# Kernel optimization log

Measured on AMD Instinct MI355X. Metric: run time of the kernel, lower is better.

Reference implementation:

```python
import jax, jax.numpy as jnp
import numpy as np

N = 524288          # number of query points
L_FREQ = 16         # frequencies in positional encoding -> dim_encoding = 3*2*16 = 96
DIM_ENC = 96
DIM_HID = 128
NUM_LAYERS = 8      # 1 input layer + 7 hidden layers + 1 output layer
DIM_OUT = 4
DIM_IN_HID = DIM_HID + DIM_ENC  # concat skip: 224


def setup_inputs() -> dict:
    key = jax.random.key(0)
    ks = jax.random.split(key, 7)
    def lin(k, fan_in, shape):
        return jax.random.uniform(k, shape, jnp.float32, -1.0, 1.0) / np.sqrt(fan_in)
    return {
        "query_points": jax.random.uniform(ks[0], (N, 3), jnp.float32),
        "W0": lin(ks[1], DIM_ENC, (DIM_ENC, DIM_HID)),
        "b0": lin(ks[2], DIM_ENC, (DIM_HID,)),
        "Wh": lin(ks[3], DIM_IN_HID, (NUM_LAYERS - 1, DIM_IN_HID, DIM_HID)),
        "bh": lin(ks[4], DIM_IN_HID, (NUM_LAYERS - 1, DIM_HID)),
        "Wl": lin(ks[5], DIM_IN_HID, (DIM_IN_HID, DIM_OUT)),
        "bl": lin(ks[6], DIM_IN_HID, (DIM_OUT,)),
    }


def _encode(x):
    # NeRF frequency encoding: [N,3] -> [N, 3*2*L_FREQ]
    freqs = (2.0 ** jnp.arange(L_FREQ, dtype=x.dtype)) * jnp.pi
    xf = x[..., None] * freqs                      # [N, 3, L]
    enc = jnp.concatenate([jnp.sin(xf), jnp.cos(xf)], axis=-1)  # [N, 3, 2L]
    return enc.reshape(x.shape[0], -1)             # [N, 96]


def reference(query_points, W0, b0, Wh, bh, Wl, bl):
    enc = _encode(query_points)                    # [N, 96]
    outs = jnp.maximum(enc @ W0 + b0, 0.0)         # [N, 128]
    outs = jnp.concatenate([outs, enc], axis=-1)   # concat skip -> [N, 224]
    for i in range(Wh.shape[0]):                   # 7 structurally-distinct hidden layers
        outs = jnp.maximum(outs @ Wh[i] + bh[i], 0.0)
        outs = jnp.concatenate([outs, enc], axis=-1)
    return outs @ Wl + bl                          # [N, 4], no activation on last layer
```

## Files before the change

### kernel.cpp

```cpp
#include <hip/hip_runtime.h>
#include <stdint.h>

typedef unsigned short u16;
typedef __bf16 bf16x8 __attribute__((ext_vector_type(8)));
typedef float f32x4 __attribute__((ext_vector_type(4)));
typedef unsigned int u32;

#define IMG_L0 0
#define IMG_H(l) (16384 + ((l)-1) * 32768)
#define IMG_OUT 245760
#define IMG_TOTAL 249856

__device__ inline int sinv(int q) {
    int s = q >> 5, gg = (q >> 3) & 3, u = (q >> 2) & 1, t = q & 3;
    return 16 * (2 * s + u) + 4 * gg + t;
}
__device__ inline int encmap(int q) {
    int c = q >> 5, gg = (q >> 3) & 3, u = (q >> 2) & 1, t = q & 3;
    int trig = gg >> 1, freq = 8 * (gg & 1) + 4 * u + t;
    return c * 32 + trig * 16 + freq;
}
__device__ inline u16 b16rne(float v) {
    u32 u = __builtin_bit_cast(u32, v);
    u += 0x7FFFu + ((u >> 16) & 1u);
    return (u16)(u >> 16);
}

__global__ void nf_prep(const float* __restrict__ W0, const float* __restrict__ b0,
                        const float* __restrict__ Wh, const float* __restrict__ bh,
                        const float* __restrict__ Wl, const float* __restrict__ bl,
                        u16* __restrict__ img) {
    int idx = blockIdx.x * 256 + threadIdx.x;
    if (idx >= IMG_TOTAL) return;
    int kpos, i, R, base;
    float v;
    if (idx < 16384) {
        kpos = idx >> 7; i = idx & 127; R = 128; base = IMG_L0;
        v = (kpos < 96) ? W0[encmap(kpos) * 128 + i]
          : (kpos == 96) ? b0[i] : 0.f;
    } else if (idx < IMG_OUT) {
        int r = idx - 16384; int l = r >> 15; int rr = r & 32767;
        kpos = rr >> 7; i = rr & 127; R = 128; base = 16384 + l * 32768;
        const float* W = Wh + l * 224 * 128;
        v = (kpos < 128) ? W[sinv(kpos) * 128 + i]
          : (kpos < 224) ? W[(128 + encmap(kpos - 128)) * 128 + i]
          : (kpos == 224) ? bh[l * 128 + i] : 0.f;
    } else {
        int r = idx - IMG_OUT; kpos = r >> 4; i = r & 15; R = 16; base = IMG_OUT;
        v = 0.f;
        if (i < 4) {
            v = (kpos < 128) ? Wl[sinv(kpos) * 4 + i]
              : (kpos < 224) ? Wl[(128 + encmap(kpos - 128)) * 4 + i]
              : (kpos == 224) ? bl[i] : 0.f;
        }
    }
    img[base + (((kpos >> 3) * R + i) << 3) + (kpos & 7)] = b16rne(v);
}

__device__ inline f32x4 MF(bf16x8 a, bf16x8 b, f32x4 c) {
    return __builtin_amdgcn_mfma_f32_16x16x32_bf16(a, b, c, 0, 0, 0);
}
__device__ inline bf16x8 fr4(const u32 (&p)[4]) {
    union { u32 u[4]; bf16x8 v; } x;
    x.u[0] = p[0]; x.u[1] = p[1]; x.u[2] = p[2]; x.u[3] = p[3];
    return x.v;
}
__device__ inline bf16x8 frCB(u32 c0) {
    union { u32 u[4]; bf16x8 v; } x;
    x.u[0] = c0; x.u[1] = 0; x.u[2] = 0; x.u[3] = 0;
    return x.v;
}
__device__ inline bf16x8 ldA(const u16* base, int gi) {
    union { uint4 q; bf16x8 v; } x;
    x.q = *(const uint4*)(base + (gi << 3));
    return x.v;
}
__device__ inline u32 pkbf(float a, float b) {
    u32 ua = __builtin_bit_cast(u32, a) + 0x8000u;
    u32 ub = __builtin_bit_cast(u32, b) + 0x8000u;
    return __builtin_amdgcn_perm(ub, ua, 0x07060302u);
}
__device__ inline void stageA(const u16* gsrc, u16* ldst, int bytes, int wave, int lane) {
    const char* gs = (const char*)gsrc + lane * 16;
    char* ls = (char*)ldst;
    for (int c = wave * 1024; c < bytes; c += 8192)
        __builtin_amdgcn_global_load_lds(
            (const __attribute__((address_space(1))) void*)(gs + c),
            (__attribute__((address_space(3))) void*)(ls + c), 16, 0, 0);
}
__device__ inline void zeroacc(f32x4 (&acc)[8][2]) {
#pragma unroll
    for (int T = 0; T < 8; T++) {
        acc[T][0] = f32x4{0.f, 0.f, 0.f, 0.f};
        acc[T][1] = f32x4{0.f, 0.f, 0.f, 0.f};
    }
}
__device__ inline void buildH(const f32x4 (&acc)[8][2], u32 (&H)[2][4][4]) {
#pragma unroll
    for (int n = 0; n < 2; n++)
#pragma unroll
        for (int s = 0; s < 4; s++) {
            f32x4 a = acc[2 * s][n], b = acc[2 * s + 1][n];
            float a0 = fmaxf(a[0], 0.f), a1 = fmaxf(a[1], 0.f);
            float a2 = fmaxf(a[2], 0.f), a3 = fmaxf(a[3], 0.f);
            float c0 = fmaxf(b[0], 0.f), c1 = fmaxf(b[1], 0.f);
            float c2 = fmaxf(b[2], 0.f), c3 = fmaxf(b[3], 0.f);
            H[n][s][0] = pkbf(a0, a1); H[n][s][1] = pkbf(a2, a3);
            H[n][s][2] = pkbf(c0, c1); H[n][s][3] = pkbf(c2, c3);
        }
}
template <int HALF>
__device__ inline void compute_l0(const u16* A, int g, int m, f32x4 (&acc)[8][2],
                                  const u32 (&E)[2][3][4], u32 CB0) {
#pragma unroll
    for (int sr = 0; sr < 2; sr++) {
        const int s = HALF * 2 + sr;
        bf16x8 B0, B1;
        if (s < 3) { B0 = fr4(E[0][s]); B1 = fr4(E[1][s]); }
        else       { B0 = frCB(CB0);    B1 = B0; }
#pragma unroll
        for (int T = 0; T < 8; T++) {
            bf16x8 a = ldA(A, (4 * sr + g) * 128 + 16 * T + m);
            acc[T][0] = MF(a, B0, acc[T][0]);
            acc[T][1] = MF(a, B1, acc[T][1]);
        }
    }
}
template <int HALF>
__device__ inline void compute_half(const u16* A, int g, int m, f32x4 (&acc)[8][2],
                                    const u32 (&H)[2][4][4], const u32 (&E)[2][3][4],
                                    u32 CB0) {
#pragma unroll
    for (int sr = 0; sr < 4; sr++) {
        const int s = HALF * 4 + sr;
        bf16x8 B0, B1;
        if (s < 4)      { B0 = fr4(H[0][s]);     B1 = fr4(H[1][s]); }
        else if (s < 7) { B0 = fr4(E[0][s - 4]); B1 = fr4(E[1][s - 4]); }
        else            { B0 = frCB(CB0);        B1 = B0; }
#pragma unroll
        for (int T = 0; T < 8; T++) {
            bf16x8 a = ldA(A, (4 * sr + g) * 128 + 16 * T + m);
            acc[T][0] = MF(a, B0, acc[T][0]);
            acc[T][1] = MF(a, B1, acc[T][1]);
        }
    }
}

__global__ __launch_bounds__(512, 2) void nf_main(const float* __restrict__ qp,
                                                  const u16* __restrict__ img,
                                                  float* __restrict__ out) {
    __shared__ alignas(16) u16 lds[2][16384];
    const int tid = threadIdx.x, wave = tid >> 6, lane = tid & 63;
    const int m = lane & 15, g = lane >> 4;
    const int pbase = blockIdx.x * 256 + wave * 32;

    stageA(img + IMG_L0, &lds[0][0], 16384, wave, lane);

    float xs[2][3];
#pragma unroll
    for (int c = 0; c < 3; c++) {
        xs[0][c] = qp[(pbase + m) * 3 + c];
        xs[1][c] = qp[(pbase + 16 + m) * 3 + c];
    }
    u32 E[2][3][4];
    const float sc0 = (g & 1) ? 128.0f : 0.5f;
    const bool iscos = (g & 2);
#pragma unroll
    for (int n = 0; n < 2; n++)
#pragma unroll
        for (int c = 0; c < 3; c++) {
            float r = xs[n][c] * sc0;
            float v[8];
#pragma unroll
            for (int t = 0; t < 8; t++) {
                float fr = __builtin_amdgcn_fractf(r);
                v[t] = iscos ? __builtin_amdgcn_cosf(fr) : __builtin_amdgcn_sinf(fr);
                r = r * 2.0f;
            }
            E[n][c][0] = pkbf(v[0], v[1]); E[n][c][1] = pkbf(v[2], v[3]);
            E[n][c][2] = pkbf(v[4], v[5]); E[n][c][3] = pkbf(v[6], v[7]);
        }
    const u32 CB0 = (g == 0) ? 0x00003F80u : 0u;
    f32x4 acc[8][2];
    u32 H[2][4][4];
    zeroacc(acc);

    __syncthreads();
    stageA(img + IMG_L0 + 8192, &lds[1][0], 16384, wave, lane);
    compute_l0<0>(&lds[0][0], g, m, acc, E, CB0);
    __syncthreads();
    stageA(img + IMG_H(1), &lds[0][0], 32768, wave, lane);
    compute_l0<1>(&lds[1][0], g, m, acc, E, CB0);
    buildH(acc, H);
    __syncthreads();

#pragma unroll 1
    for (int l = 1; l < 8; l++) {
        const int ibase = IMG_H(l);
        stageA(img + ibase + 16384, &lds[1][0], 32768, wave, lane);
        zeroacc(acc);
        compute_half<0>(&lds[0][0], g, m, acc, H, E, CB0);
        __syncthreads();
        const u16* nsrc = (l < 7) ? (img + ibase + 32768) : (img + IMG_OUT);
        stageA(nsrc, &lds[0][0], (l < 7) ? 32768 : 8192, wave, lane);
        compute_half<1>(&lds[1][0], g, m, acc, H, E, CB0);
        buildH(acc, H);
        __syncthreads();
    }

    f32x4 o0 = {0.f, 0.f, 0.f, 0.f}, o1 = {0.f, 0.f, 0.f, 0.f};
#pragma unroll
    for (int s = 0; s < 8; s++) {
        bf16x8 B0, B1;
        if (s < 4)      { B0 = fr4(H[0][s]);     B1 = fr4(H[1][s]); }
        else if (s < 7) { B0 = fr4(E[0][s - 4]); B1 = fr4(E[1][s - 4]); }
        else            { B0 = frCB(CB0);        B1 = B0; }
        bf16x8 a = ldA(&lds[0][0], (4 * s + g) * 16 + m);
        o0 = MF(a, B0, o0);
        o1 = MF(a, B1, o1);
    }
    if (g == 0) {
        *(f32x4*)(out + 4 * (pbase + m))      = o0;
        *(f32x4*)(out + 4 * (pbase + 16 + m)) = o1;
    }
}

extern "C" void kernel_launch(void* const* d_in, const int* in_sizes, int n_in,
                              void* d_out, int out_size, void* d_ws, size_t ws_size,
                              hipStream_t stream) {
    const float* qp = (const float*)d_in[0];
    const float* W0 = (const float*)d_in[1];
    const float* b0 = (const float*)d_in[2];
    const float* Wh = (const float*)d_in[3];
    const float* bh = (const float*)d_in[4];
    const float* Wl = (const float*)d_in[5];
    const float* bl = (const float*)d_in[6];
    float* out = (float*)d_out;
    u16* img = (u16*)d_ws;

    nf_prep<<<976, 256, 0, stream>>>(W0, b0, Wh, bh, Wl, bl, img);
    nf_main<<<2048, 512, 0, stream>>>(qp, img, out);
}
```

Before: 308.8 us.

## Double per-wave point tile and recompute encoding instead of caching it

Each wave now handles 64 points (four 16-point MFMA tiles) instead of 32, and blocks shrink to 4 waves of 256 threads, so every weight fragment read from LDS feeds twice as many MFMAs. To keep register pressure in check, the encoding fragments are no longer held in registers. They are recomputed with sin/cos for every layer. The trade is more transcendental ALU work and more accumulator registers in exchange for half the LDS traffic per MFMA and more weight staging per wave.

```diff
diff --git a/kernel.cpp b/kernel.cpp
--- a/kernel.cpp
+++ b/kernel.cpp
@@ -5,6 +5,8 @@
 typedef __bf16 bf16x8 __attribute__((ext_vector_type(8)));
 typedef float f32x4 __attribute__((ext_vector_type(4)));
 typedef unsigned int u32;
+
+#define NT 4
 
 #define IMG_L0 0
 #define IMG_H(l) (16384 + ((l)-1) * 32768)
@@ -80,117 +82,140 @@
     u32 ub = __builtin_bit_cast(u32, b) + 0x8000u;
     return __builtin_amdgcn_perm(ub, ua, 0x07060302u);
 }
+__device__ inline bf16x8 encFrag(float x, float sc0, bool iscos) {
+    float r = x * sc0;
+    float v[8];
+#pragma unroll
+    for (int t = 0; t < 8; t++) {
+        float fr = __builtin_amdgcn_fractf(r);
+        v[t] = iscos ? __builtin_amdgcn_cosf(fr) : __builtin_amdgcn_sinf(fr);
+        r = r * 2.0f;
+    }
+    union { u32 u[4]; bf16x8 v; } o;
+    o.u[0] = pkbf(v[0], v[1]); o.u[1] = pkbf(v[2], v[3]);
+    o.u[2] = pkbf(v[4], v[5]); o.u[3] = pkbf(v[6], v[7]);
+    return o.v;
+}
 __device__ inline void stageA(const u16* gsrc, u16* ldst, int bytes, int wave, int lane) {
     const char* gs = (const char*)gsrc + lane * 16;
     char* ls = (char*)ldst;
-    for (int c = wave * 1024; c < bytes; c += 8192)
+    for (int c = wave * 1024; c < bytes; c += 4096)
         __builtin_amdgcn_global_load_lds(
             (const __attribute__((address_space(1))) void*)(gs + c),
             (__attribute__((address_space(3))) void*)(ls + c), 16, 0, 0);
 }
-__device__ inline void zeroacc(f32x4 (&acc)[8][2]) {
-#pragma unroll
-    for (int T = 0; T < 8; T++) {
-        acc[T][0] = f32x4{0.f, 0.f, 0.f, 0.f};
-        acc[T][1] = f32x4{0.f, 0.f, 0.f, 0.f};
-    }
-}
-__device__ inline void buildH(const f32x4 (&acc)[8][2], u32 (&H)[2][4][4]) {
-#pragma unroll
-    for (int n = 0; n < 2; n++)
+__device__ inline void zeroacc(f32x4 (&acc)[8][NT]) {
+#pragma unroll
+    for (int T = 0; T < 8; T++)
+#pragma unroll
+        for (int n = 0; n < NT; n++)
+            acc[T][n] = f32x4{0.f, 0.f, 0.f, 0.f};
+}
+__device__ inline void buildH(const f32x4 (&acc)[8][NT], u32 (&H)[NT][4][4]) {
+#pragma unroll
+    for (int n = 0; n < NT; n++)
 #pragma unroll
         for (int s = 0; s < 4; s++) {
             f32x4 a = acc[2 * s][n], b = acc[2 * s + 1][n];
-            float a0 = fmaxf(a[0], 0.f), a1 = fmaxf(a[1], 0.f);
-            float a2 = fmaxf(a[2], 0.f), a3 = fmaxf(a[3], 0.f);
-            float c0 = fmaxf(b[0], 0.f), c1 = fmaxf(b[1], 0.f);
-            float c2 = fmaxf(b[2], 0.f), c3 = fmaxf(b[3], 0.f);
-            H[n][s][0] = pkbf(a0, a1); H[n][s][1] = pkbf(a2, a3);
-            H[n][s][2] = pkbf(c0, c1); H[n][s][3] = pkbf(c2, c3);
+            H[n][s][0] = pkbf(fmaxf(a[0], 0.f), fmaxf(a[1], 0.f));
+            H[n][s][1] = pkbf(fmaxf(a[2], 0.f), fmaxf(a[3], 0.f));
+            H[n][s][2] = pkbf(fmaxf(b[0], 0.f), fmaxf(b[1], 0.f));
+            H[n][s][3] = pkbf(fmaxf(b[2], 0.f), fmaxf(b[3], 0.f));
         }
 }
 template <int HALF>
-__device__ inline void compute_l0(const u16* A, int g, int m, f32x4 (&acc)[8][2],
-                                  const u32 (&E)[2][3][4], u32 CB0) {
+__device__ inline void computeL0(const u16* A, int g, int m, f32x4 (&acc)[8][NT],
+                                 const float (&xs)[NT][3], float sc0, bool iscos,
+                                 u32 CB0) {
 #pragma unroll
     for (int sr = 0; sr < 2; sr++) {
         const int s = HALF * 2 + sr;
-        bf16x8 B0, B1;
-        if (s < 3) { B0 = fr4(E[0][s]); B1 = fr4(E[1][s]); }
-        else       { B0 = frCB(CB0);    B1 = B0; }
+        bf16x8 B[NT];
+        if (s < 3) {
+#pragma unroll
+            for (int n = 0; n < NT; n++) B[n] = encFrag(xs[n][s], sc0, iscos);
+        } else {
+            bf16x8 cb = frCB(CB0);
+#pragma unroll
+            for (int n = 0; n < NT; n++) B[n] = cb;
+        }
 #pragma unroll
         for (int T = 0; T < 8; T++) {
             bf16x8 a = ldA(A, (4 * sr + g) * 128 + 16 * T + m);
-            acc[T][0] = MF(a, B0, acc[T][0]);
-            acc[T][1] = MF(a, B1, acc[T][1]);
-        }
-    }
-}
-template <int HALF>
-__device__ inline void compute_half(const u16* A, int g, int m, f32x4 (&acc)[8][2],
-                                    const u32 (&H)[2][4][4], const u32 (&E)[2][3][4],
-                                    u32 CB0) {
+#pragma unroll
+            for (int n = 0; n < NT; n++) acc[T][n] = MF(a, B[n], acc[T][n]);
+        }
+    }
+}
+__device__ inline void computeHalf0(const u16* A, int g, int m, f32x4 (&acc)[8][NT],
+                                    const u32 (&H)[NT][4][4]) {
 #pragma unroll
     for (int sr = 0; sr < 4; sr++) {
-        const int s = HALF * 4 + sr;
-        bf16x8 B0, B1;
-        if (s < 4)      { B0 = fr4(H[0][s]);     B1 = fr4(H[1][s]); }
-        else if (s < 7) { B0 = fr4(E[0][s - 4]); B1 = fr4(E[1][s - 4]); }
-        else            { B0 = frCB(CB0);        B1 = B0; }
+        bf16x8 B[NT];
+#pragma unroll
+        for (int n = 0; n < NT; n++) B[n] = fr4(H[n][sr]);
 #pragma unroll
         for (int T = 0; T < 8; T++) {
             bf16x8 a = ldA(A, (4 * sr + g) * 128 + 16 * T + m);
-            acc[T][0] = MF(a, B0, acc[T][0]);
-            acc[T][1] = MF(a, B1, acc[T][1]);
-        }
-    }
-}
-
-__global__ __launch_bounds__(512, 2) void nf_main(const float* __restrict__ qp,
+#pragma unroll
+            for (int n = 0; n < NT; n++) acc[T][n] = MF(a, B[n], acc[T][n]);
+        }
+    }
+}
+__device__ inline void computeHalf1(const u16* A, int g, int m, f32x4 (&acc)[8][NT],
+                                    const float (&xs)[NT][3], float sc0, bool iscos,
+                                    u32 CB0) {
+#pragma unroll
+    for (int sr = 0; sr < 4; sr++) {
+        bf16x8 B[NT];
+        if (sr < 3) {
+#pragma unroll
+            for (int n = 0; n < NT; n++) B[n] = encFrag(xs[n][sr], sc0, iscos);
+        } else {
+            bf16x8 cb = frCB(CB0);
+#pragma unroll
+            for (int n = 0; n < NT; n++) B[n] = cb;
+        }
+#pragma unroll
+        for (int T = 0; T < 8; T++) {
+            bf16x8 a = ldA(A, (4 * sr + g) * 128 + 16 * T + m);
+#pragma unroll
+            for (int n = 0; n < NT; n++) acc[T][n] = MF(a, B[n], acc[T][n]);
+        }
+    }
+}
+
+__global__ __launch_bounds__(256, 2) void nf_main(const float* __restrict__ qp,
                                                   const u16* __restrict__ img,
                                                   float* __restrict__ out) {
     __shared__ alignas(16) u16 lds[2][16384];
     const int tid = threadIdx.x, wave = tid >> 6, lane = tid & 63;
     const int m = lane & 15, g = lane >> 4;
-    const int pbase = blockIdx.x * 256 + wave * 32;
+    const int pbase = blockIdx.x * 256 + wave * 64;
 
     stageA(img + IMG_L0, &lds[0][0], 16384, wave, lane);
 
-    float xs[2][3];
-#pragma unroll
-    for (int c = 0; c < 3; c++) {
-        xs[0][c] = qp[(pbase + m) * 3 + c];
-        xs[1][c] = qp[(pbase + 16 + m) * 3 + c];
-    }
-    u32 E[2][3][4];
+    float xs[NT][3];
+#pragma unroll
+    for (int n = 0; n < NT; n++)
+#pragma unroll
+        for (int c = 0; c < 3; c++)
+            xs[n][c] = qp[(pbase + n * 16 + m) * 3 + c];
+
     const float sc0 = (g & 1) ? 128.0f : 0.5f;
     const bool iscos = (g & 2);
-#pragma unroll
-    for (int n = 0; n < 2; n++)
-#pragma unroll
-        for (int c = 0; c < 3; c++) {
-            float r = xs[n][c] * sc0;
-            float v[8];
-#pragma unroll
-            for (int t = 0; t < 8; t++) {
-                float fr = __builtin_amdgcn_fractf(r);
-                v[t] = iscos ? __builtin_amdgcn_cosf(fr) : __builtin_amdgcn_sinf(fr);
-                r = r * 2.0f;
-            }
-            E[n][c][0] = pkbf(v[0], v[1]); E[n][c][1] = pkbf(v[2], v[3]);
-            E[n][c][2] = pkbf(v[4], v[5]); E[n][c][3] = pkbf(v[6], v[7]);
-        }
     const u32 CB0 = (g == 0) ? 0x00003F80u : 0u;
-    f32x4 acc[8][2];
-    u32 H[2][4][4];
+
+    f32x4 acc[8][NT];
+    u32 H[NT][4][4];
     zeroacc(acc);
 
     __syncthreads();
     stageA(img + IMG_L0 + 8192, &lds[1][0], 16384, wave, lane);
-    compute_l0<0>(&lds[0][0], g, m, acc, E, CB0);
+    computeL0<0>(&lds[0][0], g, m, acc, xs, sc0, iscos, CB0);
     __syncthreads();
     stageA(img + IMG_H(1), &lds[0][0], 32768, wave, lane);
-    compute_l0<1>(&lds[1][0], g, m, acc, E, CB0);
+    computeL0<1>(&lds[1][0], g, m, acc, xs, sc0, iscos, CB0);
     buildH(acc, H);
     __syncthreads();
 
@@ -199,29 +224,40 @@
         const int ibase = IMG_H(l);
         stageA(img + ibase + 16384, &lds[1][0], 32768, wave, lane);
         zeroacc(acc);
-        compute_half<0>(&lds[0][0], g, m, acc, H, E, CB0);
+        computeHalf0(&lds[0][0], g, m, acc, H);
         __syncthreads();
         const u16* nsrc = (l < 7) ? (img + ibase + 32768) : (img + IMG_OUT);
         stageA(nsrc, &lds[0][0], (l < 7) ? 32768 : 8192, wave, lane);
-        compute_half<1>(&lds[1][0], g, m, acc, H, E, CB0);
+        computeHalf1(&lds[1][0], g, m, acc, xs, sc0, iscos, CB0);
         buildH(acc, H);
         __syncthreads();
     }
 
-    f32x4 o0 = {0.f, 0.f, 0.f, 0.f}, o1 = {0.f, 0.f, 0.f, 0.f};
+    f32x4 o[NT];
+#pragma unroll
+    for (int n = 0; n < NT; n++) o[n] = f32x4{0.f, 0.f, 0.f, 0.f};
 #pragma unroll
     for (int s = 0; s < 8; s++) {
-        bf16x8 B0, B1;
-        if (s < 4)      { B0 = fr4(H[0][s]);     B1 = fr4(H[1][s]); }
-        else if (s < 7) { B0 = fr4(E[0][s - 4]); B1 = fr4(E[1][s - 4]); }
-        else            { B0 = frCB(CB0);        B1 = B0; }
+        bf16x8 B[NT];
+        if (s < 4) {
+#pragma unroll
+            for (int n = 0; n < NT; n++) B[n] = fr4(H[n][s]);
+        } else if (s < 7) {
+#pragma unroll
+            for (int n = 0; n < NT; n++) B[n] = encFrag(xs[n][s - 4], sc0, iscos);
+        } else {
+            bf16x8 cb = frCB(CB0);
+#pragma unroll
+            for (int n = 0; n < NT; n++) B[n] = cb;
+        }
         bf16x8 a = ldA(&lds[0][0], (4 * s + g) * 16 + m);
-        o0 = MF(a, B0, o0);
-        o1 = MF(a, B1, o1);
+#pragma unroll
+        for (int n = 0; n < NT; n++) o[n] = MF(a, B[n], o[n]);
     }
     if (g == 0) {
-        *(f32x4*)(out + 4 * (pbase + m))      = o0;
-        *(f32x4*)(out + 4 * (pbase + 16 + m)) = o1;
+#pragma unroll
+        for (int n = 0; n < NT; n++)
+            *(f32x4*)(out + 4 * (pbase + n * 16 + m)) = o[n];
     }
 }
 
@@ -239,5 +275,5 @@
     u16* img = (u16*)d_ws;
 
     nf_prep<<<976, 256, 0, stream>>>(W0, b0, Wh, bh, Wl, bl, img);
-    nf_main<<<2048, 512, 0, stream>>>(qp, img, out);
-}
+    nf_main<<<2048, 256, 0, stream>>>(qp, img, out);
+}
```

After: 267.1 us. -13.5%, faster.

## Switch MLP to 32x32x16 MFMA with 64-point waves and tighter weight image

Applied to the files above, without the earlier changes.

Replaces the 16x16x32 bf16 MFMA tiling with 32x32x16 MFMA, so each wave handles 64 points and blocks shrink to 256 threads. Each lane now computes both sin and cos for its encoding slice. The weight image is repacked with a new K-permutation that drops padding rows (224+bias instead of 256 per layer). The aim is to cut LDS A-operand reads per FLOP and wasted K padding, at the cost of more accumulator registers and fewer waves per block.

```diff
diff --git a/kernel.cpp b/kernel.cpp
--- a/kernel.cpp
+++ b/kernel.cpp
@@ -4,21 +4,16 @@
 typedef unsigned short u16;
 typedef __bf16 bf16x8 __attribute__((ext_vector_type(8)));
 typedef float f32x4 __attribute__((ext_vector_type(4)));
+typedef float f32x16 __attribute__((ext_vector_type(16)));
 typedef unsigned int u32;
 
-#define IMG_L0 0
-#define IMG_H(l) (16384 + ((l)-1) * 32768)
-#define IMG_OUT 245760
-#define IMG_TOTAL 249856
-
-__device__ inline int sinv(int q) {
-    int s = q >> 5, gg = (q >> 3) & 3, u = (q >> 2) & 1, t = q & 3;
-    return 16 * (2 * s + u) + 4 * gg + t;
-}
-__device__ inline int encmap(int q) {
-    int c = q >> 5, gg = (q >> 3) & 3, u = (q >> 2) & 1, t = q & 3;
-    int trig = gg >> 1, freq = 8 * (gg & 1) + 4 * u + t;
-    return c * 32 + trig * 16 + freq;
+#define IMG_H(l) (14336 + ((l)-1) * 30720)
+#define IMG_OUT 229376
+#define IMG_TOTAL 237056
+
+__device__ inline int fmap(int k) {
+    int s = k >> 4, h = (k >> 3) & 1, j = k & 7;
+    return 32 * (s >> 1) + 16 * (s & 1) + 8 * (j >> 2) + 4 * h + (j & 3);
 }
 __device__ inline u16 b16rne(float v) {
     u32 u = __builtin_bit_cast(u32, v);
@@ -32,33 +27,35 @@
                         u16* __restrict__ img) {
     int idx = blockIdx.x * 256 + threadIdx.x;
     if (idx >= IMG_TOTAL) return;
-    int kpos, i, R, base;
     float v;
-    if (idx < 16384) {
-        kpos = idx >> 7; i = idx & 127; R = 128; base = IMG_L0;
-        v = (kpos < 96) ? W0[encmap(kpos) * 128 + i]
-          : (kpos == 96) ? b0[i] : 0.f;
+    if (idx < 14336) {
+        int gg = idx >> 3, j = idx & 7;
+        int koct = gg >> 7, i = gg & 127, k = koct * 8 + j;
+        v = (k < 96) ? W0[k * 128 + i] : (k == 96) ? b0[i] : 0.f;
     } else if (idx < IMG_OUT) {
-        int r = idx - 16384; int l = r >> 15; int rr = r & 32767;
-        kpos = rr >> 7; i = rr & 127; R = 128; base = 16384 + l * 32768;
+        int r = idx - 14336, l = r / 30720, rr = r % 30720;
+        int gg = rr >> 3, j = rr & 7;
+        int koct = gg >> 7, i = gg & 127, k = koct * 8 + j;
         const float* W = Wh + l * 224 * 128;
-        v = (kpos < 128) ? W[sinv(kpos) * 128 + i]
-          : (kpos < 224) ? W[(128 + encmap(kpos - 128)) * 128 + i]
-          : (kpos == 224) ? bh[l * 128 + i] : 0.f;
+        v = (k < 128) ? W[fmap(k) * 128 + i]
+          : (k < 224) ? W[k * 128 + i]
+          : (k == 224) ? bh[l * 128 + i] : 0.f;
     } else {
-        int r = idx - IMG_OUT; kpos = r >> 4; i = r & 15; R = 16; base = IMG_OUT;
+        int r = idx - IMG_OUT;
+        int gg = r >> 3, j = r & 7;
+        int koct = gg >> 5, i = gg & 31, k = koct * 8 + j;
         v = 0.f;
-        if (i < 4) {
-            v = (kpos < 128) ? Wl[sinv(kpos) * 4 + i]
-              : (kpos < 224) ? Wl[(128 + encmap(kpos - 128)) * 4 + i]
-              : (kpos == 224) ? bl[i] : 0.f;
-        }
-    }
-    img[base + (((kpos >> 3) * R + i) << 3) + (kpos & 7)] = b16rne(v);
-}
-
-__device__ inline f32x4 MF(bf16x8 a, bf16x8 b, f32x4 c) {
-    return __builtin_amdgcn_mfma_f32_16x16x32_bf16(a, b, c, 0, 0, 0);
+        if (i < 4)
+            v = (k < 128) ? Wl[fmap(k) * 4 + i]
+              : (k < 224) ? Wl[k * 4 + i]
+              : (k == 224) ? bl[i] : 0.f;
+    }
+    img[idx & 7 ? idx : idx] = 0;
+    img[idx] = b16rne(v);
+}
+
+__device__ inline f32x16 MF32(bf16x8 a, bf16x8 b, f32x16 c) {
+    return __builtin_amdgcn_mfma_f32_32x32x16_bf16(a, b, c, 0, 0, 0);
 }
 __device__ inline bf16x8 fr4(const u32 (&p)[4]) {
     union { u32 u[4]; bf16x8 v; } x;
@@ -83,145 +80,159 @@
 __device__ inline void stageA(const u16* gsrc, u16* ldst, int bytes, int wave, int lane) {
     const char* gs = (const char*)gsrc + lane * 16;
     char* ls = (char*)ldst;
-    for (int c = wave * 1024; c < bytes; c += 8192)
+    for (int c = wave * 1024; c < bytes; c += 4096)
         __builtin_amdgcn_global_load_lds(
             (const __attribute__((address_space(1))) void*)(gs + c),
             (__attribute__((address_space(3))) void*)(ls + c), 16, 0, 0);
 }
-__device__ inline void zeroacc(f32x4 (&acc)[8][2]) {
-#pragma unroll
-    for (int T = 0; T < 8; T++) {
-        acc[T][0] = f32x4{0.f, 0.f, 0.f, 0.f};
-        acc[T][1] = f32x4{0.f, 0.f, 0.f, 0.f};
-    }
-}
-__device__ inline void buildH(const f32x4 (&acc)[8][2], u32 (&H)[2][4][4]) {
+__device__ inline void zeroacc(f32x16 (&acc)[4][2]) {
+#pragma unroll
+    for (int t = 0; t < 4; t++)
+#pragma unroll
+        for (int n = 0; n < 2; n++)
+#pragma unroll
+            for (int r = 0; r < 16; r++) acc[t][n][r] = 0.f;
+}
+__device__ inline void buildH(const f32x16 (&acc)[4][2], u32 (&H)[2][8][4]) {
 #pragma unroll
     for (int n = 0; n < 2; n++)
 #pragma unroll
-        for (int s = 0; s < 4; s++) {
-            f32x4 a = acc[2 * s][n], b = acc[2 * s + 1][n];
-            float a0 = fmaxf(a[0], 0.f), a1 = fmaxf(a[1], 0.f);
-            float a2 = fmaxf(a[2], 0.f), a3 = fmaxf(a[3], 0.f);
-            float c0 = fmaxf(b[0], 0.f), c1 = fmaxf(b[1], 0.f);
-            float c2 = fmaxf(b[2], 0.f), c3 = fmaxf(b[3], 0.f);
-            H[n][s][0] = pkbf(a0, a1); H[n][s][1] = pkbf(a2, a3);
-            H[n][s][2] = pkbf(c0, c1); H[n][s][3] = pkbf(c2, c3);
-        }
-}
-template <int HALF>
-__device__ inline void compute_l0(const u16* A, int g, int m, f32x4 (&acc)[8][2],
-                                  const u32 (&E)[2][3][4], u32 CB0) {
-#pragma unroll
-    for (int sr = 0; sr < 2; sr++) {
-        const int s = HALF * 2 + sr;
+        for (int s = 0; s < 8; s++) {
+            const int t = s >> 1, rb = (s & 1) * 8;
+#pragma unroll
+            for (int q = 0; q < 4; q++)
+                H[n][s][q] = pkbf(fmaxf(acc[t][n][rb + 2 * q], 0.f),
+                                  fmaxf(acc[t][n][rb + 2 * q + 1], 0.f));
+        }
+}
+__device__ inline void cHid0(const u16* A, int h, int m32, f32x16 (&acc)[4][2],
+                             const u32 (&H)[2][8][4]) {
+#pragma unroll
+    for (int s = 0; s < 8; s++) {
+        bf16x8 B0 = fr4(H[0][s]), B1 = fr4(H[1][s]);
+#pragma unroll
+        for (int t = 0; t < 4; t++) {
+            bf16x8 a = ldA(A, (2 * s + h) * 128 + t * 32 + m32);
+            acc[t][0] = MF32(a, B0, acc[t][0]);
+            acc[t][1] = MF32(a, B1, acc[t][1]);
+        }
+    }
+}
+__device__ inline void cHid1(const u16* A, int h, int m32, f32x16 (&acc)[4][2],
+                             const u32 (&E)[2][3][2][4], u32 CB0) {
+#pragma unroll
+    for (int s = 0; s < 7; s++) {
         bf16x8 B0, B1;
-        if (s < 3) { B0 = fr4(E[0][s]); B1 = fr4(E[1][s]); }
-        else       { B0 = frCB(CB0);    B1 = B0; }
-#pragma unroll
-        for (int T = 0; T < 8; T++) {
-            bf16x8 a = ldA(A, (4 * sr + g) * 128 + 16 * T + m);
-            acc[T][0] = MF(a, B0, acc[T][0]);
-            acc[T][1] = MF(a, B1, acc[T][1]);
-        }
-    }
-}
-template <int HALF>
-__device__ inline void compute_half(const u16* A, int g, int m, f32x4 (&acc)[8][2],
-                                    const u32 (&H)[2][4][4], const u32 (&E)[2][3][4],
-                                    u32 CB0) {
-#pragma unroll
-    for (int sr = 0; sr < 4; sr++) {
-        const int s = HALF * 4 + sr;
-        bf16x8 B0, B1;
-        if (s < 4)      { B0 = fr4(H[0][s]);     B1 = fr4(H[1][s]); }
-        else if (s < 7) { B0 = fr4(E[0][s - 4]); B1 = fr4(E[1][s - 4]); }
-        else            { B0 = frCB(CB0);        B1 = B0; }
-#pragma unroll
-        for (int T = 0; T < 8; T++) {
-            bf16x8 a = ldA(A, (4 * sr + g) * 128 + 16 * T + m);
-            acc[T][0] = MF(a, B0, acc[T][0]);
-            acc[T][1] = MF(a, B1, acc[T][1]);
-        }
-    }
-}
-
-__global__ __launch_bounds__(512, 2) void nf_main(const float* __restrict__ qp,
+        if (s < 6) { B0 = fr4(E[0][s >> 1][s & 1]); B1 = fr4(E[1][s >> 1][s & 1]); }
+        else       { B0 = frCB(CB0); B1 = B0; }
+#pragma unroll
+        for (int t = 0; t < 4; t++) {
+            bf16x8 a = ldA(A, (2 * s + h) * 128 + t * 32 + m32);
+            acc[t][0] = MF32(a, B0, acc[t][0]);
+            acc[t][1] = MF32(a, B1, acc[t][1]);
+        }
+    }
+}
+
+__global__ __launch_bounds__(256, 2) void nf_main(const float* __restrict__ qp,
                                                   const u16* __restrict__ img,
                                                   float* __restrict__ out) {
     __shared__ alignas(16) u16 lds[2][16384];
     const int tid = threadIdx.x, wave = tid >> 6, lane = tid & 63;
-    const int m = lane & 15, g = lane >> 4;
-    const int pbase = blockIdx.x * 256 + wave * 32;
-
-    stageA(img + IMG_L0, &lds[0][0], 16384, wave, lane);
-
-    float xs[2][3];
-#pragma unroll
-    for (int c = 0; c < 3; c++) {
-        xs[0][c] = qp[(pbase + m) * 3 + c];
-        xs[1][c] = qp[(pbase + 16 + m) * 3 + c];
-    }
-    u32 E[2][3][4];
-    const float sc0 = (g & 1) ? 128.0f : 0.5f;
-    const bool iscos = (g & 2);
+    const int m32 = lane & 31, h = lane >> 5;
+    const int pbase = blockIdx.x * 256 + wave * 64;
+
+    stageA(img, &lds[0][0], 16384, wave, lane);
+
+    u32 E[2][3][2][4];
+    const float sc0 = h ? 128.0f : 0.5f;
 #pragma unroll
     for (int n = 0; n < 2; n++)
 #pragma unroll
         for (int c = 0; c < 3; c++) {
-            float r = xs[n][c] * sc0;
-            float v[8];
+            float r = qp[(pbase + n * 32 + m32) * 3 + c] * sc0;
+            float sn[8], cs[8];
 #pragma unroll
             for (int t = 0; t < 8; t++) {
                 float fr = __builtin_amdgcn_fractf(r);
-                v[t] = iscos ? __builtin_amdgcn_cosf(fr) : __builtin_amdgcn_sinf(fr);
+                sn[t] = __builtin_amdgcn_sinf(fr);
+                cs[t] = __builtin_amdgcn_cosf(fr);
                 r = r * 2.0f;
             }
-            E[n][c][0] = pkbf(v[0], v[1]); E[n][c][1] = pkbf(v[2], v[3]);
-            E[n][c][2] = pkbf(v[4], v[5]); E[n][c][3] = pkbf(v[6], v[7]);
-        }
-    const u32 CB0 = (g == 0) ? 0x00003F80u : 0u;
-    f32x4 acc[8][2];
-    u32 H[2][4][4];
+#pragma unroll
+            for (int q = 0; q < 4; q++) {
+                E[n][c][0][q] = pkbf(sn[2 * q], sn[2 * q + 1]);
+                E[n][c][1][q] = pkbf(cs[2 * q], cs[2 * q + 1]);
+            }
+        }
+    const u32 CB0 = (h == 0) ? 0x00003F80u : 0u;
+
+    f32x16 acc[4][2];
+    u32 H[2][8][4];
     zeroacc(acc);
 
     __syncthreads();
-    stageA(img + IMG_L0 + 8192, &lds[1][0], 16384, wave, lane);
-    compute_l0<0>(&lds[0][0], g, m, acc, E, CB0);
+    stageA(img + 8192, &lds[1][0], 12288, wave, lane);
+#pragma unroll
+    for (int s = 0; s < 4; s++) {
+        bf16x8 B0 = fr4(E[0][s >> 1][s & 1]), B1 = fr4(E[1][s >> 1][s & 1]);
+#pragma unroll
+        for (int t = 0; t < 4; t++) {
+            bf16x8 a = ldA(&lds[0][0], (2 * s + h) * 128 + t * 32 + m32);
+            acc[t][0] = MF32(a, B0, acc[t][0]);
+            acc[t][1] = MF32(a, B1, acc[t][1]);
+        }
+    }
     __syncthreads();
     stageA(img + IMG_H(1), &lds[0][0], 32768, wave, lane);
-    compute_l0<1>(&lds[1][0], g, m, acc, E, CB0);
+#pragma unroll
+    for (int s = 0; s < 3; s++) {
+        bf16x8 B0, B1;
+        if (s < 2) { B0 = fr4(E[0][2][s]); B1 = fr4(E[1][2][s]); }
+        else       { B0 = frCB(CB0); B1 = B0; }
+#pragma unroll
+        for (int t = 0; t < 4; t++) {
+            bf16x8 a = ldA(&lds[1][0], (2 * s + h) * 128 + t * 32 + m32);
+            acc[t][0] = MF32(a, B0, acc[t][0]);
+            acc[t][1] = MF32(a, B1, acc[t][1]);
+        }
+    }
     buildH(acc, H);
     __syncthreads();
 
 #pragma unroll 1
     for (int l = 1; l < 8; l++) {
-        const int ibase = IMG_H(l);
-        stageA(img + ibase + 16384, &lds[1][0], 32768, wave, lane);
+        const int base = IMG_H(l);
+        stageA(img + base + 16384, &lds[1][0], 28672, wave, lane);
         zeroacc(acc);
-        compute_half<0>(&lds[0][0], g, m, acc, H, E, CB0);
+        cHid0(&lds[0][0], h, m32, acc, H);
         __syncthreads();
-        const u16* nsrc = (l < 7) ? (img + ibase + 32768) : (img + IMG_OUT);
-        stageA(nsrc, &lds[0][0], (l < 7) ? 32768 : 8192, wave, lane);
-        compute_half<1>(&lds[1][0], g, m, acc, H, E, CB0);
+        const u16* nsrc = (l < 7) ? (img + base + 30720) : (img + IMG_OUT);
+        stageA(nsrc, &lds[0][0], (l < 7) ? 32768 : 15360, wave, lane);
+        cHid1(&lds[1][0], h, m32, acc, E, CB0);
         buildH(acc, H);
         __syncthreads();
     }
 
-    f32x4 o0 = {0.f, 0.f, 0.f, 0.f}, o1 = {0.f, 0.f, 0.f, 0.f};
-#pragma unroll
-    for (int s = 0; s < 8; s++) {
+    f32x16 o0, o1;
+#pragma unroll
+    for (int r = 0; r < 16; r++) { o0[r] = 0.f; o1[r] = 0.f; }
+#pragma unroll
+    for (int s = 0; s < 15; s++) {
         bf16x8 B0, B1;
-        if (s < 4)      { B0 = fr4(H[0][s]);     B1 = fr4(H[1][s]); }
-        else if (s < 7) { B0 = fr4(E[0][s - 4]); B1 = fr4(E[1][s - 4]); }
-        else            { B0 = frCB(CB0);        B1 = B0; }
-        bf16x8 a = ldA(&lds[0][0], (4 * s + g) * 16 + m);
-        o0 = MF(a, B0, o0);
-        o1 = MF(a, B1, o1);
-    }
-    if (g == 0) {
-        *(f32x4*)(out + 4 * (pbase + m))      = o0;
-        *(f32x4*)(out + 4 * (pbase + 16 + m)) = o1;
+        if (s < 8)       { B0 = fr4(H[0][s]); B1 = fr4(H[1][s]); }
+        else if (s < 14) { B0 = fr4(E[0][(s - 8) >> 1][(s - 8) & 1]);
+                           B1 = fr4(E[1][(s - 8) >> 1][(s - 8) & 1]); }
+        else             { B0 = frCB(CB0); B1 = B0; }
+        bf16x8 a = ldA(&lds[0][0], (2 * s + h) * 32 + m32);
+        o0 = MF32(a, B0, o0);
+        o1 = MF32(a, B1, o1);
+    }
+    if (h == 0) {
+        f32x4 w0 = {o0[0], o0[1], o0[2], o0[3]};
+        f32x4 w1 = {o1[0], o1[1], o1[2], o1[3]};
+        *(f32x4*)(out + 4 * (pbase + m32)) = w0;
+        *(f32x4*)(out + 4 * (pbase + 32 + m32)) = w1;
     }
 }
 
@@ -238,6 +249,6 @@
     float* out = (float*)d_out;
     u16* img = (u16*)d_ws;
 
-    nf_prep<<<976, 256, 0, stream>>>(W0, b0, Wh, bh, Wl, bl, img);
-    nf_main<<<2048, 512, 0, stream>>>(qp, img, out);
-}
+    nf_prep<<<926, 256, 0, stream>>>(W0, b0, Wh, bh, Wl, bl, img);
+    nf_main<<<2048, 256, 0, stream>>>(qp, img, out);
+}
```

Result: faster. 262.3 us (-15.1%).
